# Kernel optimization log

Hardware: AMD Instinct MI355X
Metric: run time of the kernel (lower is better)

Reference implementation:

```python
import jax, jax.numpy as jnp
import numpy as np
import math

D_MODEL = 2048
N_HEADS = 32
N_KV_HEADS = 8
HEAD_DIM = D_MODEL // N_HEADS  # 64
N_GROUPS = N_HEADS // N_KV_HEADS  # 4
MAX_SEQ_LEN = 2048
ROPE_THETA = 500000.0


def precompute_rope(head_dim, max_seq_len, theta=ROPE_THETA):
    freqs = 1.0 / theta ** (jnp.arange(0, head_dim, 2, dtype=jnp.float32) / head_dim)
    positions = jnp.arange(max_seq_len, dtype=jnp.float32)
    angles = jnp.outer(positions, freqs)  # [S, head_dim/2]
    return jnp.cos(angles), jnp.sin(angles)


def apply_rope(x, cos, sin):
    # x: [B, H, S, D]; cos/sin: [S, D/2]
    half = x.shape[-1] // 2
    x1, x2 = x[..., :half], x[..., half:]
    cos = cos[None, None]
    sin = sin[None, None]
    return jnp.concatenate([x1 * cos - x2 * sin, x1 * sin + x2 * cos], axis=-1)


def setup_inputs() -> dict:
    key = jax.random.key(0)
    k1, k2, k3, k4, k5 = jax.random.split(key, 5)
    B, S = 2, 2048
    x = jax.random.normal(k1, (B, S, D_MODEL), dtype=jnp.float32)
    sd = 1.0 / math.sqrt(D_MODEL)
    # weights stored as [in, out] so forward is x @ W (same math as torch Linear)
    W_q = jax.random.normal(k2, (D_MODEL, N_HEADS * HEAD_DIM), dtype=jnp.float32) * sd
    W_k = jax.random.normal(k3, (D_MODEL, N_KV_HEADS * HEAD_DIM), dtype=jnp.float32) * sd
    W_v = jax.random.normal(k4, (D_MODEL, N_KV_HEADS * HEAD_DIM), dtype=jnp.float32) * sd
    W_o = jax.random.normal(k5, (N_HEADS * HEAD_DIM, D_MODEL), dtype=jnp.float32) * sd
    cos, sin = precompute_rope(HEAD_DIM, MAX_SEQ_LEN)
    return {"x": x, "W_q": W_q, "W_k": W_k, "W_v": W_v, "W_o": W_o,
            "rope_cos": cos, "rope_sin": sin}


def reference(x, W_q, W_k, W_v, W_o, rope_cos, rope_sin):
    B, S, _ = x.shape
    scale = 1.0 / math.sqrt(HEAD_DIM)
    # projections -> [B, H, S, D]
    q = (x @ W_q).reshape(B, S, N_HEADS, HEAD_DIM).transpose(0, 2, 1, 3)
    k = (x @ W_k).reshape(B, S, N_KV_HEADS, HEAD_DIM).transpose(0, 2, 1, 3)
    v = (x @ W_v).reshape(B, S, N_KV_HEADS, HEAD_DIM).transpose(0, 2, 1, 3)
    # RoPE
    q = apply_rope(q, rope_cos[:S], rope_sin[:S])
    k = apply_rope(k, rope_cos[:S], rope_sin[:S])
    # GQA expand: repeat each KV head n_groups times
    k = jnp.repeat(k, N_GROUPS, axis=1)  # [B, H, S, D]
    v = jnp.repeat(v, N_GROUPS, axis=1)
    # scores + causal mask + softmax
    scores = jnp.einsum('bhqd,bhkd->bhqk', q, k) * scale
    causal = jnp.tril(jnp.ones((S, S), dtype=bool))
    scores = jnp.where(causal[None, None], scores, -jnp.inf)
    weights = jax.nn.softmax(scores, axis=-1)
    attn_out = jnp.einsum('bhqk,bhkd->bhqd', weights, v)
    out = attn_out.transpose(0, 2, 1, 3).reshape(B, S, N_HEADS * HEAD_DIM) @ W_o
    return out
```

## Files before the change

kernel.cpp:

```cpp
#include <hip/hip_runtime.h>
#include <hip/hip_bf16.h>

typedef __attribute__((ext_vector_type(8))) short short8;
typedef __attribute__((ext_vector_type(4))) short short4v;
typedef __attribute__((ext_vector_type(4))) float f32x4;

#define MFMA(A,B,C) __builtin_amdgcn_mfma_f32_16x16x32_bf16(A,B,C,0,0,0)
#define SW(row) ((((row) & 3)) | (((row) >> 1) & 4))
#define SCL 0.18033688f

__device__ __forceinline__ short f2bs(float f) {
    __hip_bfloat16 h = __float2bfloat16(f);
    union { __hip_bfloat16 h; short s; } u; u.h = h; return u.s;
}

__device__ __forceinline__ float exp2v(float x) {
    float r; asm("v_exp_f32 %0, %1" : "=v"(r) : "v"(x)); return r;
}

__device__ __forceinline__ void async16(void* lds, const void* g) {
    __builtin_amdgcn_global_load_lds(
        (const __attribute__((address_space(1))) unsigned int*)g,
        (__attribute__((address_space(3))) unsigned int*)lds, 16, 0, 0);
}

__global__ __launch_bounds__(256) void cast_bf16_k(const float* __restrict__ X,
                                                   short* __restrict__ Y, int n4) {
    int i = blockIdx.x * 256 + threadIdx.x;
    if (i >= n4) return;
    const float4 v = *(const float4*)(X + (size_t)i * 4);
    short4v o;
    o.x = f2bs(v.x); o.y = f2bs(v.y); o.z = f2bs(v.z); o.w = f2bs(v.w);
    *(short4v*)(Y + (size_t)i * 4) = o;
}

__global__ __launch_bounds__(256) void transpose_cast_k(const float* __restrict__ W,
                                                        short* __restrict__ Wt, int K, int N) {
    __shared__ float tile[32][33];
    int n0 = blockIdx.x * 32, k0 = blockIdx.y * 32;
    int tx = threadIdx.x, ty = threadIdx.y;
    #pragma unroll
    for (int i = 0; i < 32; i += 8)
        tile[ty + i][tx] = W[(size_t)(k0 + ty + i) * N + n0 + tx];
    __syncthreads();
    #pragma unroll
    for (int i = 0; i < 32; i += 8)
        Wt[(size_t)(n0 + ty + i) * K + k0 + tx] = f2bs(tile[tx][ty + i]);
}

__global__ __launch_bounds__(512, 2) void gemm_k(
    const short* __restrict__ A, const short* __restrict__ Bt,
    float* __restrict__ Cf, short* __restrict__ Cq, short* __restrict__ Ck,
    short* __restrict__ Cv,
    const float* __restrict__ rc, const float* __restrict__ rs,
    int M, int N, int K, int epi)
{
    extern __shared__ short lds[];
    const int t = threadIdx.x;
    const int l = t & 63, w = t >> 6;
    const int lo = l & 15, hi = l >> 4;
    const int wm = w >> 1, wn = w & 1;
    const int tm = blockIdx.x * 256, tn = blockIdx.y * 128;
    const int lr = l >> 3, ls = l & 7;

    const f32x4 z4 = {0.f, 0.f, 0.f, 0.f};
    f32x4 acc[4][4];
    #pragma unroll
    for (int m = 0; m < 4; ++m)
        #pragma unroll
        for (int n = 0; n < 4; ++n) acc[m][n] = z4;

    auto stage = [&](int kt, int buf) {
        const size_t ko = (size_t)kt * 64;
        short* Abuf = lds + buf * 24576;
        short* Bbuf = Abuf + 16384;
        #pragma unroll
        for (int j = 0; j < 4; ++j) {
            int g = w * 4 + j;
            int row = g * 8 + lr;
            int gs = ls ^ SW(row);
            async16(Abuf + g * 512, A + (size_t)(tm + row) * K + ko + gs * 8);
        }
        #pragma unroll
        for (int j = 0; j < 2; ++j) {
            int g = w * 2 + j;
            int row = g * 8 + lr;
            int gs = ls ^ SW(row);
            async16(Bbuf + g * 512, Bt + (size_t)(tn + row) * K + ko + gs * 8);
        }
    };

    const int nkt = K >> 6;
    stage(0, 0);
    if (nkt > 1) stage(1, 1);

    int buf = 0;
    for (int kt = 0; kt < nkt; ++kt) {
        if (kt + 1 < nkt) asm volatile("s_waitcnt vmcnt(6)" ::: "memory");
        else              asm volatile("s_waitcnt vmcnt(0)" ::: "memory");
        __builtin_amdgcn_s_barrier();
        if (kt + 2 < nkt) {
            int tb = buf - 1; if (tb < 0) tb = 2;
            stage(kt + 2, tb);
        }
        const short* Ab_ = lds + buf * 24576;
        const short* Bb_ = Ab_ + 16384;
        #pragma unroll
        for (int ks = 0; ks < 2; ++ks) {
            const int slot = ks * 4 + hi;
            short8 af[4], bfr[4];
            #pragma unroll
            for (int m = 0; m < 4; ++m) {
                int row = wm * 64 + m * 16 + lo;
                af[m] = *(const short8*)(Ab_ + row * 64 + ((slot ^ SW(row)) << 3));
            }
            #pragma unroll
            for (int n = 0; n < 4; ++n) {
                int row = wn * 64 + n * 16 + lo;
                bfr[n] = *(const short8*)(Bb_ + row * 64 + ((slot ^ SW(row)) << 3));
            }
            __builtin_amdgcn_s_setprio(1);
            #pragma unroll
            for (int m = 0; m < 4; ++m)
                #pragma unroll
                for (int n = 0; n < 4; ++n)
                    acc[m][n] = MFMA(af[m], bfr[n], acc[m][n]);
            __builtin_amdgcn_s_setprio(0);
        }
        buf = (buf == 2) ? 0 : buf + 1;
    }

    if (epi == 0) {
        #pragma unroll
        for (int m = 0; m < 4; ++m)
            #pragma unroll
            for (int r = 0; r < 4; ++r) {
                int row = tm + wm * 64 + m * 16 + hi * 4 + r;
                #pragma unroll
                for (int n = 0; n < 4; ++n) {
                    int col = tn + wn * 64 + n * 16 + lo;
                    Cf[(size_t)row * N + col] = acc[m][n][r];
                }
            }
    } else {
        const int ctn = tn + wn * 64;
        if (ctn < 2048) {
            #pragma unroll
            for (int m = 0; m < 4; ++m)
                #pragma unroll
                for (int r = 0; r < 4; ++r) {
                    int row = tm + wm * 64 + m * 16 + hi * 4 + r;
                    int b = row >> 11, s = row & 2047;
                    #pragma unroll
                    for (int n = 0; n < 2; ++n) {
                        int col = ctn + n * 16 + lo;
                        int h = col >> 6, d = col & 63;
                        float x1 = acc[m][n][r], x2 = acc[m][n + 2][r];
                        float c = rc[s * 32 + d], sn = rs[s * 32 + d];
                        size_t base = (((size_t)b * 32 + h) * 2048 + s) * 64;
                        Cq[base + d]      = f2bs((x1 * c - x2 * sn) * SCL);
                        Cq[base + d + 32] = f2bs((x1 * sn + x2 * c) * SCL);
                    }
                }
        } else if (ctn < 2560) {
            #pragma unroll
            for (int m = 0; m < 4; ++m)
                #pragma unroll
                for (int r = 0; r < 4; ++r) {
                    int row = tm + wm * 64 + m * 16 + hi * 4 + r;
                    int b = row >> 11, s = row & 2047;
                    #pragma unroll
                    for (int n = 0; n < 2; ++n) {
                        int col = ctn - 2048 + n * 16 + lo;
                        int h = col >> 6, d = col & 63;
                        float x1 = acc[m][n][r], x2 = acc[m][n + 2][r];
                        float c = rc[s * 32 + d], sn = rs[s * 32 + d];
                        size_t base = (((size_t)b * 8 + h) * 2048 + s) * 64;
                        Ck[base + d]      = f2bs(x1 * c - x2 * sn);
                        Ck[base + d + 32] = f2bs(x1 * sn + x2 * c);
                    }
                }
        } else {
            #pragma unroll
            for (int m = 0; m < 4; ++m)
                #pragma unroll
                for (int r = 0; r < 4; ++r) {
                    int row = tm + wm * 64 + m * 16 + hi * 4 + r;
                    int b = row >> 11, s = row & 2047;
                    #pragma unroll
                    for (int n = 0; n < 4; ++n) {
                        int col = ctn - 2560 + n * 16 + lo;
                        int h = col >> 6, d = col & 63;
                        Cv[(((size_t)b * 8 + h) * 64 + d) * 2048 + s] = f2bs(acc[m][n][r]);
                    }
                }
        }
    }
}

__global__ __launch_bounds__(256) void attn_k(
    const short* __restrict__ Qp, const short* __restrict__ Kp, const short* __restrict__ Vt,
    short* __restrict__ Ab)
{
    __shared__ short KV[2][8192];
    const int t = threadIdx.x, l = t & 63, w = t >> 6;
    const int lo = l & 15, hi = l >> 4;
    const int lr = l >> 3, ls = l & 7;
    const int pair = blockIdx.x;
    const int h = blockIdx.y, b = blockIdx.z;
    const int kvh = h >> 2;
    const size_t qbase  = (size_t)(b * 32 + h) * 2048 * 64;
    const size_t kbase  = (size_t)(b * 8 + kvh) * 2048 * 64;
    const size_t vtbase = (size_t)(b * 8 + kvh) * 64 * 2048;
    const size_t abase  = (size_t)b * 2048 * 2048 + (size_t)h * 64;

    for (int halfq = 0; halfq < 2; ++halfq) {
        const int qtile = halfq ? 15 - pair : pair;
        const int nkt = 2 * qtile + 2;

        short8 qf[2][2];
        #pragma unroll
        for (int g = 0; g < 2; ++g) {
            int qrow = qtile * 128 + w * 32 + g * 16 + lo;
            #pragma unroll
            for (int ks = 0; ks < 2; ++ks)
                qf[g][ks] = *(const short8*)(Qp + qbase + (size_t)qrow * 64 + (ks * 4 + hi) * 8);
        }

        const f32x4 z4 = {0.f, 0.f, 0.f, 0.f};
        float m_run[2] = {-3e38f, -3e38f};
        float l_run[2] = {0.f, 0.f};
        f32x4 oacc[2][4];
        #pragma unroll
        for (int g = 0; g < 2; ++g)
            #pragma unroll
            for (int nd = 0; nd < 4; ++nd) oacc[g][nd] = z4;

        #pragma unroll
        for (int j = 0; j < 2; ++j) {
            int g8 = w * 2 + j;
            int row = g8 * 8 + lr;
            int gs = ls ^ SW(row);
            async16(&KV[0][g8 * 512],        Kp + kbase + (size_t)row * 64 + gs * 8);
            async16(&KV[0][4096 + g8 * 512], Vt + vtbase + (size_t)row * 2048 + gs * 8);
        }
        __syncthreads();

        int cur = 0;
        for (int kt = 0; kt < nkt; ++kt) {
            if (kt + 1 < nkt) {
                #pragma unroll
                for (int j = 0; j < 2; ++j) {
                    int g8 = w * 2 + j;
                    int row = g8 * 8 + lr;
                    int gs = ls ^ SW(row);
                    async16(&KV[cur ^ 1][g8 * 512],
                            Kp + kbase + (size_t)((kt + 1) * 64 + row) * 64 + gs * 8);
                    async16(&KV[cur ^ 1][4096 + g8 * 512],
                            Vt + vtbase + (size_t)row * 2048 + (kt + 1) * 64 + gs * 8);
                }
            }

            const short* Ks = &KV[cur][0];
            const short* Vs = &KV[cur][4096];

            f32x4 sacc[2][4];
            #pragma unroll
            for (int g = 0; g < 2; ++g)
                #pragma unroll
                for (int n = 0; n < 4; ++n) sacc[g][n] = z4;
            __builtin_amdgcn_s_setprio(1);
            #pragma unroll
            for (int ks = 0; ks < 2; ++ks) {
                const int slot = ks * 4 + hi;
                #pragma unroll
                for (int n = 0; n < 4; ++n) {
                    const int krow = ((lo >> 2) << 3) + ((n & 1) << 2) + (lo & 3) + ((n >> 1) << 5);
                    short8 kf = *(const short8*)(Ks + krow * 64 + ((slot ^ SW(krow)) << 3));
                    sacc[0][n] = MFMA(kf, qf[0][ks], sacc[0][n]);
                    sacc[1][n] = MFMA(kf, qf[1][ks], sacc[1][n]);
                }
            }
            __builtin_amdgcn_s_setprio(0);

            short8 afr[2][2];
            #pragma unroll
            for (int g = 0; g < 2; ++g) {
                const int qmin = qtile * 128 + w * 32 + g * 16;
                const int q = qmin + lo;
                float p[4][4];
                float pm = -3e38f;
                if (kt * 64 + 63 > qmin) {
                    #pragma unroll
                    for (int n = 0; n < 4; ++n)
                        #pragma unroll
                        for (int r = 0; r < 4; ++r) {
                            int k = kt * 64 + hi * 8 + ((n & 1) << 2) + r + ((n >> 1) << 5);
                            float sv = (k > q) ? -3e38f : sacc[g][n][r];
                            p[n][r] = sv;
                            pm = fmaxf(pm, sv);
                        }
                } else {
                    #pragma unroll
                    for (int n = 0; n < 4; ++n)
                        #pragma unroll
                        for (int r = 0; r < 4; ++r) {
                            p[n][r] = sacc[g][n][r];
                            pm = fmaxf(pm, p[n][r]);
                        }
                }
                pm = fmaxf(pm, __shfl_xor(pm, 16, 64));
                pm = fmaxf(pm, __shfl_xor(pm, 32, 64));
                if (!__all(pm <= m_run[g] + 8.f)) {
                    float mn = fmaxf(m_run[g], pm);
                    float al = exp2v(m_run[g] - mn);
                    m_run[g] = mn;
                    l_run[g] *= al;
                    float alq[4];
                    #pragma unroll
                    for (int r = 0; r < 4; ++r)
                        alq[r] = __shfl(al, (l & 48) | (hi * 4 + r), 64);
                    #pragma unroll
                    for (int nd = 0; nd < 4; ++nd) {
                        oacc[g][nd][0] *= alq[0]; oacc[g][nd][1] *= alq[1];
                        oacc[g][nd][2] *= alq[2]; oacc[g][nd][3] *= alq[3];
                    }
                }
                float rsum = 0.f;
                #pragma unroll
                for (int n = 0; n < 4; ++n)
                    #pragma unroll
                    for (int r = 0; r < 4; ++r) {
                        float e = exp2v(p[n][r] - m_run[g]);
                        p[n][r] = e;
                        rsum += e;
                    }
                rsum += __shfl_xor(rsum, 16, 64);
                rsum += __shfl_xor(rsum, 32, 64);
                l_run[g] += rsum;
                #pragma unroll
                for (int ks = 0; ks < 2; ++ks) {
                    short8 a;
                    a[0] = f2bs(p[2 * ks][0]);     a[1] = f2bs(p[2 * ks][1]);
                    a[2] = f2bs(p[2 * ks][2]);     a[3] = f2bs(p[2 * ks][3]);
                    a[4] = f2bs(p[2 * ks + 1][0]); a[5] = f2bs(p[2 * ks + 1][1]);
                    a[6] = f2bs(p[2 * ks + 1][2]); a[7] = f2bs(p[2 * ks + 1][3]);
                    afr[g][ks] = a;
                }
            }

            __builtin_amdgcn_s_setprio(1);
            #pragma unroll
            for (int ks = 0; ks < 2; ++ks) {
                const int slot = ks * 4 + hi;
                #pragma unroll
                for (int nd = 0; nd < 4; ++nd) {
                    const int vrow = nd * 16 + lo;
                    short8 vf = *(const short8*)(Vs + vrow * 64 + ((slot ^ SW(vrow)) << 3));
                    oacc[0][nd] = MFMA(afr[0][ks], vf, oacc[0][nd]);
                    oacc[1][nd] = MFMA(afr[1][ks], vf, oacc[1][nd]);
                }
            }
            __builtin_amdgcn_s_setprio(0);

            __syncthreads();
            cur ^= 1;
        }

        #pragma unroll
        for (int g = 0; g < 2; ++g) {
            float rl[4];
            #pragma unroll
            for (int r = 0; r < 4; ++r)
                rl[r] = 1.0f / __shfl(l_run[g], (l & 48) | (hi * 4 + r), 64);
            #pragma unroll
            for (int nd = 0; nd < 4; ++nd)
                #pragma unroll
                for (int r = 0; r < 4; ++r) {
                    int s = qtile * 128 + w * 32 + g * 16 + hi * 4 + r;
                    Ab[abase + (size_t)s * 2048 + nd * 16 + lo] = f2bs(oacc[g][nd][r] * rl[r]);
                }
        }
    }
}

extern "C" void kernel_launch(void* const* d_in, const int* in_sizes, int n_in,
                              void* d_out, int out_size, void* d_ws, size_t ws_size,
                              hipStream_t stream)
{
    const float* x  = (const float*)d_in[0];
    const float* Wq = (const float*)d_in[1];
    const float* Wk = (const float*)d_in[2];
    const float* Wv = (const float*)d_in[3];
    const float* Wo = (const float*)d_in[4];
    const float* rc = (const float*)d_in[5];
    const float* rs = (const float*)d_in[6];
    float* out = (float*)d_out;
    char* ws = (char*)d_ws;

    size_t off = 0;
    short* x_bf   = (short*)(ws + off); off += (size_t)4096 * 2048 * 2;
    short* Wqkv_t = (short*)(ws + off); off += (size_t)3072 * 2048 * 2;
    short* Wo_t   = (short*)(ws + off); off += (size_t)2048 * 2048 * 2;
    short* Qp     = (short*)(ws + off); off += (size_t)2 * 32 * 2048 * 64 * 2;
    short* Kp     = (short*)(ws + off); off += (size_t)2 * 8 * 2048 * 64 * 2;
    short* Vtb    = (short*)(ws + off); off += (size_t)2 * 8 * 64 * 2048 * 2;
    short* Ab     = (short*)(ws + off); off += (size_t)4096 * 2048 * 2;
    if (off > ws_size) return;

    const int LDS_BYTES = 3 * 24576 * 2;
    (void)hipFuncSetAttribute((const void*)gemm_k,
                              hipFuncAttributeMaxDynamicSharedMemorySize, LDS_BYTES);

    cast_bf16_k<<<8192, 256, 0, stream>>>(x, x_bf, 2097152);
    transpose_cast_k<<<dim3(64, 64), dim3(32, 8), 0, stream>>>(Wq, Wqkv_t, 2048, 2048);
    transpose_cast_k<<<dim3(16, 64), dim3(32, 8), 0, stream>>>(Wk, Wqkv_t + (size_t)2048 * 2048, 2048, 512);
    transpose_cast_k<<<dim3(16, 64), dim3(32, 8), 0, stream>>>(Wv, Wqkv_t + (size_t)2560 * 2048, 2048, 512);
    transpose_cast_k<<<dim3(64, 64), dim3(32, 8), 0, stream>>>(Wo, Wo_t, 2048, 2048);

    gemm_k<<<dim3(16, 24), 512, LDS_BYTES, stream>>>(x_bf, Wqkv_t, nullptr, Qp, Kp, Vtb,
                                                     rc, rs, 4096, 3072, 2048, 4);

    attn_k<<<dim3(8, 32, 2), 256, 0, stream>>>(Qp, Kp, Vtb, Ab);

    gemm_k<<<dim3(16, 16), 512, LDS_BYTES, stream>>>(Ab, Wo_t, out, nullptr, nullptr, nullptr,
                                                     nullptr, nullptr, 4096, 2048, 2048, 0);
}
```

Measured before the change: 194.8 us.

## Interleave split global-to-LDS prefetch with MFMA phases in GEMM main loop

Restructures the projection GEMM K-loop into four phases, each loading a subset of A/B fragments from LDS and issuing part of the next-next tile's async global-to-LDS loads before running an MFMA cluster. Barriers and explicit lgkmcnt/vmcnt waits with sched_barrier enforce a fixed schedule, so memory issue is spread across the compute phases instead of bunched at the iteration start. The cost is many more workgroup barriers per iteration, which can stall waves, plus tighter reliance on the hand-tuned vmcnt counts staying correct.

```diff
diff --git a/kernel.cpp b/kernel.cpp
--- a/kernel.cpp
+++ b/kernel.cpp
@@ -70,17 +70,20 @@
         #pragma unroll
         for (int n = 0; n < 4; ++n) acc[m][n] = z4;
 
-    auto stage = [&](int kt, int buf) {
+    auto stageA = [&](int kt, int buf, int j0) {
         const size_t ko = (size_t)kt * 64;
         short* Abuf = lds + buf * 24576;
-        short* Bbuf = Abuf + 16384;
-        #pragma unroll
-        for (int j = 0; j < 4; ++j) {
-            int g = w * 4 + j;
+        #pragma unroll
+        for (int j = 0; j < 2; ++j) {
+            int g = w * 4 + j0 + j;
             int row = g * 8 + lr;
             int gs = ls ^ SW(row);
             async16(Abuf + g * 512, A + (size_t)(tm + row) * K + ko + gs * 8);
         }
+    };
+    auto stageB = [&](int kt, int buf) {
+        const size_t ko = (size_t)kt * 64;
+        short* Bbuf = lds + buf * 24576 + 16384;
         #pragma unroll
         for (int j = 0; j < 2; ++j) {
             int g = w * 2 + j;
@@ -91,43 +94,108 @@
     };
 
     const int nkt = K >> 6;
-    stage(0, 0);
-    if (nkt > 1) stage(1, 1);
+    stageA(0, 0, 0); stageA(0, 0, 2); stageB(0, 0);
+    stageA(1, 1, 0); stageA(1, 1, 2); stageB(1, 1);
+    asm volatile("s_waitcnt vmcnt(6)" ::: "memory");
+    __builtin_amdgcn_s_barrier();
 
     int buf = 0;
     for (int kt = 0; kt < nkt; ++kt) {
-        if (kt + 1 < nkt) asm volatile("s_waitcnt vmcnt(6)" ::: "memory");
-        else              asm volatile("s_waitcnt vmcnt(0)" ::: "memory");
-        __builtin_amdgcn_s_barrier();
-        if (kt + 2 < nkt) {
-            int tb = buf - 1; if (tb < 0) tb = 2;
-            stage(kt + 2, tb);
-        }
         const short* Ab_ = lds + buf * 24576;
         const short* Bb_ = Ab_ + 16384;
-        #pragma unroll
-        for (int ks = 0; ks < 2; ++ks) {
-            const int slot = ks * 4 + hi;
-            short8 af[4], bfr[4];
-            #pragma unroll
-            for (int m = 0; m < 4; ++m) {
-                int row = wm * 64 + m * 16 + lo;
-                af[m] = *(const short8*)(Ab_ + row * 64 + ((slot ^ SW(row)) << 3));
-            }
+        const int nb = (buf == 2) ? 0 : buf + 1;
+        const int pb = (nb == 2) ? 0 : nb + 1;
+        const bool pf = (kt + 2 < nkt);
+        short8 af0, af1, bfr[4];
+
+        {
+            const int slot = hi;
+            { int row = wm * 64 + lo;
+              af0 = *(const short8*)(Ab_ + row * 64 + ((slot ^ SW(row)) << 3)); }
+            { int row = wm * 64 + 16 + lo;
+              af1 = *(const short8*)(Ab_ + row * 64 + ((slot ^ SW(row)) << 3)); }
             #pragma unroll
             for (int n = 0; n < 4; ++n) {
                 int row = wn * 64 + n * 16 + lo;
                 bfr[n] = *(const short8*)(Bb_ + row * 64 + ((slot ^ SW(row)) << 3));
             }
-            __builtin_amdgcn_s_setprio(1);
-            #pragma unroll
-            for (int m = 0; m < 4; ++m)
-                #pragma unroll
-                for (int n = 0; n < 4; ++n)
-                    acc[m][n] = MFMA(af[m], bfr[n], acc[m][n]);
-            __builtin_amdgcn_s_setprio(0);
-        }
-        buf = (buf == 2) ? 0 : buf + 1;
+            if (pf) stageA(kt + 2, pb, 0);
+            __builtin_amdgcn_s_barrier();
+            asm volatile("s_waitcnt lgkmcnt(0)" ::: "memory");
+            __builtin_amdgcn_sched_barrier(0);
+            __builtin_amdgcn_s_setprio(1);
+            #pragma unroll
+            for (int n = 0; n < 4; ++n) {
+                acc[0][n] = MFMA(af0, bfr[n], acc[0][n]);
+                acc[1][n] = MFMA(af1, bfr[n], acc[1][n]);
+            }
+            __builtin_amdgcn_s_setprio(0);
+            __builtin_amdgcn_s_barrier();
+        }
+        {
+            const int slot = hi;
+            { int row = wm * 64 + 32 + lo;
+              af0 = *(const short8*)(Ab_ + row * 64 + ((slot ^ SW(row)) << 3)); }
+            { int row = wm * 64 + 48 + lo;
+              af1 = *(const short8*)(Ab_ + row * 64 + ((slot ^ SW(row)) << 3)); }
+            if (pf) stageA(kt + 2, pb, 2);
+            __builtin_amdgcn_s_barrier();
+            asm volatile("s_waitcnt lgkmcnt(0)" ::: "memory");
+            __builtin_amdgcn_sched_barrier(0);
+            __builtin_amdgcn_s_setprio(1);
+            #pragma unroll
+            for (int n = 0; n < 4; ++n) {
+                acc[2][n] = MFMA(af0, bfr[n], acc[2][n]);
+                acc[3][n] = MFMA(af1, bfr[n], acc[3][n]);
+            }
+            __builtin_amdgcn_s_setprio(0);
+            __builtin_amdgcn_s_barrier();
+        }
+        {
+            const int slot = 4 + hi;
+            { int row = wm * 64 + lo;
+              af0 = *(const short8*)(Ab_ + row * 64 + ((slot ^ SW(row)) << 3)); }
+            { int row = wm * 64 + 16 + lo;
+              af1 = *(const short8*)(Ab_ + row * 64 + ((slot ^ SW(row)) << 3)); }
+            #pragma unroll
+            for (int n = 0; n < 4; ++n) {
+                int row = wn * 64 + n * 16 + lo;
+                bfr[n] = *(const short8*)(Bb_ + row * 64 + ((slot ^ SW(row)) << 3));
+            }
+            if (pf) stageB(kt + 2, pb);
+            __builtin_amdgcn_s_barrier();
+            asm volatile("s_waitcnt lgkmcnt(0)" ::: "memory");
+            __builtin_amdgcn_sched_barrier(0);
+            __builtin_amdgcn_s_setprio(1);
+            #pragma unroll
+            for (int n = 0; n < 4; ++n) {
+                acc[0][n] = MFMA(af0, bfr[n], acc[0][n]);
+                acc[1][n] = MFMA(af1, bfr[n], acc[1][n]);
+            }
+            __builtin_amdgcn_s_setprio(0);
+            __builtin_amdgcn_s_barrier();
+        }
+        {
+            const int slot = 4 + hi;
+            { int row = wm * 64 + 32 + lo;
+              af0 = *(const short8*)(Ab_ + row * 64 + ((slot ^ SW(row)) << 3)); }
+            { int row = wm * 64 + 48 + lo;
+              af1 = *(const short8*)(Ab_ + row * 64 + ((slot ^ SW(row)) << 3)); }
+            __builtin_amdgcn_s_barrier();
+            asm volatile("s_waitcnt lgkmcnt(0)" ::: "memory");
+            __builtin_amdgcn_sched_barrier(0);
+            __builtin_amdgcn_s_setprio(1);
+            #pragma unroll
+            for (int n = 0; n < 4; ++n) {
+                acc[2][n] = MFMA(af0, bfr[n], acc[2][n]);
+                acc[3][n] = MFMA(af1, bfr[n], acc[3][n]);
+            }
+            __builtin_amdgcn_s_setprio(0);
+            if (pf) asm volatile("s_waitcnt vmcnt(6)" ::: "memory");
+            else    asm volatile("s_waitcnt vmcnt(0)" ::: "memory");
+            __builtin_amdgcn_s_barrier();
+        }
+        buf = nb;
     }
 
     if (epi == 0) {
```

After: 205.0 us. +5.2%, slower.

## Enlarge GEMM tile to 256x256 with double-buffered phased prefetch and XCD-aware block remap

Applied to the files above, without the earlier changes.

The GEMM tile grows from 256x128 to 256x256, with 8 waves arranged 2x4 and each wave computing 128x64. This raises arithmetic intensity per LDS load. The 3-stage buffer becomes a 2-stage double buffer, with the next tile's loads split into four quarter-stages interleaved with four MFMA phases and separated by barriers. Block IDs are also remapped round-robin across 8 groups to improve L2 locality across XCDs. In exchange the grid shrinks to 192 and 128 blocks, under one wave on 256 CUs, while register pressure from 32 accumulators and barriers per k-step both increase.

```diff
diff --git a/kernel.cpp b/kernel.cpp
--- a/kernel.cpp
+++ b/kernel.cpp
@@ -59,83 +59,88 @@
     const int t = threadIdx.x;
     const int l = t & 63, w = t >> 6;
     const int lo = l & 15, hi = l >> 4;
-    const int wm = w >> 1, wn = w & 1;
-    const int tm = blockIdx.x * 256, tn = blockIdx.y * 128;
+    const int wm = w >> 2, wn = w & 3;
     const int lr = l >> 3, ls = l & 7;
 
+    const int nbx = gridDim.x;
+    const int nwg = nbx * gridDim.y;
+    const int bid0 = blockIdx.y * nbx + blockIdx.x;
+    const int wg = (bid0 & 7) * (nwg >> 3) + (bid0 >> 3);
+    const int tm = (wg % nbx) * 256, tn = (wg / nbx) * 256;
+
     const f32x4 z4 = {0.f, 0.f, 0.f, 0.f};
-    f32x4 acc[4][4];
+    f32x4 acc[8][4];
     #pragma unroll
-    for (int m = 0; m < 4; ++m)
+    for (int m = 0; m < 8; ++m)
         #pragma unroll
         for (int n = 0; n < 4; ++n) acc[m][n] = z4;
 
-    auto stage = [&](int kt, int buf) {
+    auto stage_half = [&](int kt, int buf, int h) {
         const size_t ko = (size_t)kt * 64;
-        short* Abuf = lds + buf * 24576;
-        short* Bbuf = Abuf + 16384;
-        #pragma unroll
-        for (int j = 0; j < 4; ++j) {
-            int g = w * 4 + j;
-            int row = g * 8 + lr;
-            int gs = ls ^ SW(row);
-            async16(Abuf + g * 512, A + (size_t)(tm + row) * K + ko + gs * 8);
-        }
+        const short* src = (h < 2) ? A : Bt;
+        const int rbase = (h & 1) << 7;
+        const int gbase = (h < 2) ? tm : tn;
+        short* dst = lds + buf * 32768 + ((h < 2) ? 0 : 16384) + rbase * 64;
         #pragma unroll
         for (int j = 0; j < 2; ++j) {
             int g = w * 2 + j;
             int row = g * 8 + lr;
             int gs = ls ^ SW(row);
-            async16(Bbuf + g * 512, Bt + (size_t)(tn + row) * K + ko + gs * 8);
+            async16(dst + g * 512, src + (size_t)(gbase + rbase + row) * K + ko + gs * 8);
         }
     };
 
     const int nkt = K >> 6;
-    stage(0, 0);
-    if (nkt > 1) stage(1, 1);
-
-    int buf = 0;
+    #pragma unroll
+    for (int h = 0; h < 4; ++h) stage_half(0, 0, h);
+    __syncthreads();
+
+    int cur = 0;
     for (int kt = 0; kt < nkt; ++kt) {
-        if (kt + 1 < nkt) asm volatile("s_waitcnt vmcnt(6)" ::: "memory");
-        else              asm volatile("s_waitcnt vmcnt(0)" ::: "memory");
-        __builtin_amdgcn_s_barrier();
-        if (kt + 2 < nkt) {
-            int tb = buf - 1; if (tb < 0) tb = 2;
-            stage(kt + 2, tb);
-        }
-        const short* Ab_ = lds + buf * 24576;
+        const bool pf = (kt + 1 < nkt);
+        const short* Ab_ = lds + cur * 32768;
         const short* Bb_ = Ab_ + 16384;
-        #pragma unroll
-        for (int ks = 0; ks < 2; ++ks) {
+        short8 af[4], bfr[4];
+        #pragma unroll
+        for (int ph = 0; ph < 4; ++ph) {
+            const int ks = ph >> 1, mh = ph & 1;
             const int slot = ks * 4 + hi;
-            short8 af[4], bfr[4];
-            #pragma unroll
-            for (int m = 0; m < 4; ++m) {
-                int row = wm * 64 + m * 16 + lo;
-                af[m] = *(const short8*)(Ab_ + row * 64 + ((slot ^ SW(row)) << 3));
-            }
-            #pragma unroll
-            for (int n = 0; n < 4; ++n) {
-                int row = wn * 64 + n * 16 + lo;
-                bfr[n] = *(const short8*)(Bb_ + row * 64 + ((slot ^ SW(row)) << 3));
-            }
+            #pragma unroll
+            for (int mm = 0; mm < 4; ++mm) {
+                int row = wm * 128 + (mh * 4 + mm) * 16 + lo;
+                af[mm] = *(const short8*)(Ab_ + row * 64 + ((slot ^ SW(row)) << 3));
+            }
+            if (mh == 0) {
+                #pragma unroll
+                for (int n = 0; n < 4; ++n) {
+                    int row = wn * 64 + n * 16 + lo;
+                    bfr[n] = *(const short8*)(Bb_ + row * 64 + ((slot ^ SW(row)) << 3));
+                }
+            }
+            if (pf) stage_half(kt + 1, cur ^ 1, ph);
+            __builtin_amdgcn_s_barrier();
+            asm volatile("s_waitcnt lgkmcnt(0)" ::: "memory");
+            __builtin_amdgcn_sched_barrier(0);
             __builtin_amdgcn_s_setprio(1);
             #pragma unroll
-            for (int m = 0; m < 4; ++m)
-                #pragma unroll
-                for (int n = 0; n < 4; ++n)
-                    acc[m][n] = MFMA(af[m], bfr[n], acc[m][n]);
+            for (int n = 0; n < 4; ++n)
+                #pragma unroll
+                for (int mm = 0; mm < 4; ++mm)
+                    acc[mh * 4 + mm][n] = MFMA(af[mm], bfr[n], acc[mh * 4 + mm][n]);
             __builtin_amdgcn_s_setprio(0);
-        }
-        buf = (buf == 2) ? 0 : buf + 1;
+            if (ph == 3 && pf)
+                asm volatile("s_waitcnt vmcnt(0)" ::: "memory");
+            __builtin_amdgcn_s_barrier();
+        }
+        cur ^= 1;
     }
 
     if (epi == 0) {
         #pragma unroll
-        for (int m = 0; m < 4; ++m)
+        for (int m = 0; m < 8; ++m)
             #pragma unroll
             for (int r = 0; r < 4; ++r) {
-                int row = tm + wm * 64 + m * 16 + hi * 4 + r;
+                int row = tm + wm * 128 + m * 16 + hi * 4 + r;
                 #pragma unroll
                 for (int n = 0; n < 4; ++n) {
                     int col = tn + wn * 64 + n * 16 + lo;
@@ -146,10 +151,10 @@
         const int ctn = tn + wn * 64;
         if (ctn < 2048) {
             #pragma unroll
-            for (int m = 0; m < 4; ++m)
+            for (int m = 0; m < 8; ++m)
                 #pragma unroll
                 for (int r = 0; r < 4; ++r) {
-                    int row = tm + wm * 64 + m * 16 + hi * 4 + r;
+                    int row = tm + wm * 128 + m * 16 + hi * 4 + r;
                     int b = row >> 11, s = row & 2047;
                     #pragma unroll
                     for (int n = 0; n < 2; ++n) {
@@ -164,10 +169,10 @@
                 }
         } else if (ctn < 2560) {
             #pragma unroll
-            for (int m = 0; m < 4; ++m)
+            for (int m = 0; m < 8; ++m)
                 #pragma unroll
                 for (int r = 0; r < 4; ++r) {
-                    int row = tm + wm * 64 + m * 16 + hi * 4 + r;
+                    int row = tm + wm * 128 + m * 16 + hi * 4 + r;
                     int b = row >> 11, s = row & 2047;
                     #pragma unroll
                     for (int n = 0; n < 2; ++n) {
@@ -182,10 +187,10 @@
                 }
         } else {
             #pragma unroll
-            for (int m = 0; m < 4; ++m)
+            for (int m = 0; m < 8; ++m)
                 #pragma unroll
                 for (int r = 0; r < 4; ++r) {
-                    int row = tm + wm * 64 + m * 16 + hi * 4 + r;
+                    int row = tm + wm * 128 + m * 16 + hi * 4 + r;
                     int b = row >> 11, s = row & 2047;
                     #pragma unroll
                     for (int n = 0; n < 4; ++n) {
@@ -408,7 +413,7 @@
     short* Ab     = (short*)(ws + off); off += (size_t)4096 * 2048 * 2;
     if (off > ws_size) return;
 
-    const int LDS_BYTES = 3 * 24576 * 2;
+    const int LDS_BYTES = 2 * 32768 * 2;
     (void)hipFuncSetAttribute((const void*)gemm_k,
                               hipFuncAttributeMaxDynamicSharedMemorySize, LDS_BYTES);
 
@@ -418,11 +423,11 @@
     transpose_cast_k<<<dim3(16, 64), dim3(32, 8), 0, stream>>>(Wv, Wqkv_t + (size_t)2560 * 2048, 2048, 512);
     transpose_cast_k<<<dim3(64, 64), dim3(32, 8), 0, stream>>>(Wo, Wo_t, 2048, 2048);
 
-    gemm_k<<<dim3(16, 24), 512, LDS_BYTES, stream>>>(x_bf, Wqkv_t, nullptr, Qp, Kp, Vtb,
+    gemm_k<<<dim3(16, 12), 512, LDS_BYTES, stream>>>(x_bf, Wqkv_t, nullptr, Qp, Kp, Vtb,
                                                      rc, rs, 4096, 3072, 2048, 4);
 
     attn_k<<<dim3(8, 32, 2), 256, 0, stream>>>(Qp, Kp, Vtb, Ab);
 
-    gemm_k<<<dim3(16, 16), 512, LDS_BYTES, stream>>>(Ab, Wo_t, out, nullptr, nullptr, nullptr,
-                                                     nullptr, nullptr, 4096, 2048, 2048, 0);
-}
+    gemm_k<<<dim3(16, 8), 512, LDS_BYTES, stream>>>(Ab, Wo_t, out, nullptr, nullptr, nullptr,
+                                                    nullptr, nullptr, 4096, 2048, 2048, 0);
+}
```

New measurement: 214.2 us. 1.1x slower.
